# Kernel tuning notes

Hardware: AMD Instinct MI355X
Metric: run time of the kernel (lower is better)

## Reference

```python
import jax, jax.numpy as jnp
import numpy as np

B, SQ, SK = 2, 2048, 2048
E = 256   # embed_dim (also per-head key dim in this MHA)
S = 256   # srcdim (also per-head value dim)
NH = 8    # num_heads
HID = 2 * S  # FFN hidden = in_dim * 2


def setup_inputs() -> dict:
    key = jax.random.key(0)
    ks = jax.random.split(key, 12)
    def w(k, shape, s=0.02):
        return jax.random.normal(k, shape, dtype=jnp.float32) * s
    return {
        "Q": jax.random.normal(ks[0], (B, SQ, E), dtype=jnp.float32),
        "H": jax.random.normal(ks[1], (B, SK, E), dtype=jnp.float32),
        "A": jax.random.normal(ks[2], (B, SK, S), dtype=jnp.float32),
        # MHA params (torch Linear convention: y = x @ W.T + b)
        "wq": w(ks[3], (NH * E, E)), "bq": jnp.zeros((NH * E,), jnp.float32),
        "wk": w(ks[4], (NH * E, E)), "bk": jnp.zeros((NH * E,), jnp.float32),
        "wv": w(ks[5], (NH * S, S)), "bv": jnp.zeros((NH * S,), jnp.float32),
        "wo": w(ks[6], (S, NH * S)), "bo": jnp.zeros((S,), jnp.float32),
        # Attension scale (Parameter(torch.ones(1)))
        "attn_scale": jnp.ones((), jnp.float32),
        # shared LayerNormA params
        "ln_g": jnp.ones((S,), jnp.float32), "ln_b": jnp.zeros((S,), jnp.float32),
        # FFN params
        "w1": w(ks[7], (HID, S)), "b1": jnp.zeros((HID,), jnp.float32),
        "w2": w(ks[8], (S, HID)), "b2": jnp.zeros((S,), jnp.float32),
    }


def _layernorm(x, g, b, eps=1e-5):
    m = x.mean(-1, keepdims=True)
    v = ((x - m) ** 2).mean(-1, keepdims=True)
    return (x - m) / jnp.sqrt(v + eps) * g + b


def reference(Q, H, A, wq, bq, wk, bk, wv, bv, wo, bo,
              attn_scale, ln_g, ln_b, w1, b1, w2, b2):
    b_, sq, _ = Q.shape
    sk = H.shape[1]
    # ---- MHA branch (A_m) ----
    q = (Q @ wq.T + bq).reshape(b_, sq, NH, E).transpose(0, 2, 1, 3)  # [b,h,sq,E]
    k = (H @ wk.T + bk).reshape(b_, sk, NH, E).transpose(0, 2, 1, 3)  # [b,h,sk,E]
    v = (A @ wv.T + bv).reshape(b_, sk, NH, S).transpose(0, 2, 1, 3)  # [b,h,sk,S]
    scores = jnp.einsum('bhqe,bhke->bhqk', q, k) / jnp.sqrt(jnp.float32(E))
    probs = jax.nn.softmax(scores, axis=-1)
    ctx = jnp.einsum('bhqk,bhkd->bhqd', probs, v)          # [b,h,sq,S]
    ctx = ctx.transpose(0, 2, 1, 3).reshape(b_, sq, NH * S)
    A_m = ctx @ wo.T + bo                                   # [b,sq,S]
    # ---- Attension branch (dot score with learned scalar scale) ----
    s2 = jnp.einsum('bqe,bke->bqk', Q, H) * attn_scale      # [b,sq,sk]
    attn_out = jax.nn.softmax(s2, axis=-1) @ A              # [b,sq,S]
    # ---- residual + LN + FFN + LN (shared LayerNormA) ----
    Ad = _layernorm(A_m + attn_out, ln_g, ln_b)
    ff = jax.nn.relu(Ad @ w1.T + b1) @ w2.T + b2
    return _layernorm(ff + Ad, ln_g, ln_b)
```

## Files before the change

kernel.cpp:

```cpp
#include <hip/hip_runtime.h>
#include <cstdint>
#include <cstddef>


typedef unsigned short u16;
typedef __attribute__((ext_vector_type(8))) short bf16x8;
typedef __attribute__((ext_vector_type(4))) short s16x4;
typedef __attribute__((ext_vector_type(4))) float f32x4;

__device__ __forceinline__ float b2f(u16 u){
  union { unsigned int i; float f; } v; v.i = ((unsigned int)u) << 16; return v.f;
}
__device__ __forceinline__ u16 f2b(float f){
  union { float f; unsigned int i; } v; v.f = f;
  unsigned int u = v.i;
  unsigned int r = (u + 0x7FFFu + ((u >> 16) & 1u)) >> 16;
  return (u16)r;
}
__device__ __forceinline__ f32x4 mfma16(bf16x8 a, bf16x8 b, f32x4 c){
  return __builtin_amdgcn_mfma_f32_16x16x32_bf16(a, b, c, 0, 0, 0);
}
__device__ __forceinline__ void gload_lds16(const void* g, void* l){
  __builtin_amdgcn_global_load_lds(
      (const __attribute__((address_space(1))) unsigned int*)g,
      (__attribute__((address_space(3))) unsigned int*)l, 16, 0, 0);
}

__global__ void detect_kernel(const u16* __restrict__ q, int* __restrict__ flag){
  __shared__ int cnt;
  if (threadIdx.x == 0) cnt = 0;
  __syncthreads();
  int c = 0;
  for (int i = threadIdx.x; i < 2048; i += 256){
    u16 u = q[i];
    int e = (u >> 7) & 0xFF;
    if (e >= 140) c++;
  }
  atomicAdd(&cnt, c);
  __syncthreads();
  if (threadIdx.x == 0) *flag = (cnt > 64) ? 1 : 0;
}

struct ConvJobs {
  const void* src[18];
  void*       dst[18];
  void*       dst2[18];
  int         n[18];
  int         mode[18];
};

__global__ void convert_all(ConvJobs J, const int* __restrict__ flag){
  const int j = blockIdx.y;
  const int n = J.n[j];
  const int mode = J.mode[j];
  const int isf = *flag;
  for (int i = blockIdx.x * blockDim.x + threadIdx.x; i < n; i += gridDim.x * blockDim.x){
    if (mode == 2){
      float f = isf ? ((const float*)J.src[j])[i] : b2f(((const u16*)J.src[j])[i]);
      ((float*)J.dst[j])[i] = f;
    } else {
      u16 hi, lo = 0;
      if (isf){
        float f = ((const float*)J.src[j])[i];
        hi = f2b(f);
        if (mode == 1) lo = f2b(f - b2f(hi));
      } else {
        hi = ((const u16*)J.src[j])[i];
      }
      ((u16*)J.dst[j])[i] = hi;
      if (mode == 1) ((u16*)J.dst2[j])[i] = lo;
    }
  }
}

template<int STORE, bool RELU>
__global__ __launch_bounds__(256) void gemm_bt(
    const u16* __restrict__ X, const u16* __restrict__ W,
    const float* __restrict__ bias, void* __restrict__ outp,
    int M, int N, int K)
{
  __shared__ __align__(16) u16 lx[128 * 64];
  __shared__ __align__(16) u16 lw[128 * 64];
  const int tid = threadIdx.x;
  const int l = tid & 63, w = tid >> 6;
  const int lg = l >> 4, lr = l & 15;
  const int wr = w >> 1, wc = w & 1;
  const int m0 = blockIdx.x * 128;
  const int n0 = blockIdx.y * 128;

  f32x4 acc[4][4];
#pragma unroll
  for (int mi = 0; mi < 4; mi++)
#pragma unroll
    for (int ni = 0; ni < 4; ni++) acc[mi][ni] = (f32x4){0.f, 0.f, 0.f, 0.f};

  const int nkt = K >> 6;
  for (int kt = 0; kt < nkt; ++kt){
    __syncthreads();
#pragma unroll
    for (int it = 0; it < 4; ++it){
      int c = it * 256 + tid;
      int row = c >> 3, j = c & 7;
      int sj = (j ^ (row & 7)) * 8;
      const u16* gx = X + (size_t)(m0 + row) * K + kt * 64 + sj;
      gload_lds16(gx, (char*)lx + c * 16);
      const u16* gw = W + (size_t)(n0 + row) * K + kt * 64 + sj;
      gload_lds16(gw, (char*)lw + c * 16);
    }
    __syncthreads();
#pragma unroll
    for (int ks = 0; ks < 2; ++ks){
      bf16x8 af[4], bfv[4];
      const int swz = ((ks * 4 + lg) ^ (lr & 7)) * 8;
#pragma unroll
      for (int mi = 0; mi < 4; mi++)
        af[mi] = *(const bf16x8*)(lx + (wr * 64 + mi * 16 + lr) * 64 + swz);
#pragma unroll
      for (int ni = 0; ni < 4; ni++)
        bfv[ni] = *(const bf16x8*)(lw + (wc * 64 + ni * 16 + lr) * 64 + swz);
#pragma unroll
      for (int mi = 0; mi < 4; mi++)
#pragma unroll
        for (int ni = 0; ni < 4; ni++)
          acc[mi][ni] = mfma16(af[mi], bfv[ni], acc[mi][ni]);
    }
  }

#pragma unroll
  for (int mi = 0; mi < 4; mi++)
#pragma unroll
    for (int ni = 0; ni < 4; ni++){
      const int gr0 = m0 + wr * 64 + mi * 16 + lg * 4;
      const int gc  = n0 + wc * 64 + ni * 16 + lr;
      const float bv = bias ? bias[gc] : 0.f;
      if (STORE == 2){
        const int b = gr0 >> 11, sk0 = gr0 & 2047;
        const int h = gc >> 8,  d   = gc & 255;
        s16x4 pk;
#pragma unroll
        for (int r = 0; r < 4; r++){
          float v = acc[mi][ni][r] + bv;
          pk[r] = (short)f2b(v);
        }
        *(s16x4*)((u16*)outp + ((size_t)((b << 3) + h) * 256 + d) * 2048 + sk0) = pk;
      } else {
#pragma unroll
        for (int r = 0; r < 4; r++){
          float v = acc[mi][ni][r] + bv;
          if (RELU) v = fmaxf(v, 0.f);
          size_t idx = (size_t)(gr0 + r) * N + gc;
          if (STORE == 0) ((u16*)outp)[idx] = f2b(v);
          else            ((float*)outp)[idx] = v;
        }
      }
    }
}

template<int STORE, bool RELU>
__global__ __launch_bounds__(256) void gemm_bt64(
    const u16* __restrict__ X, const u16* __restrict__ W,
    const float* __restrict__ bias, void* __restrict__ outp,
    int M, int N, int K)
{
  __shared__ __align__(16) u16 lx[64 * 64];
  __shared__ __align__(16) u16 lw[64 * 64];
  const int tid = threadIdx.x;
  const int l = tid & 63, w = tid >> 6;
  const int lg = l >> 4, lr = l & 15;
  const int wr = w >> 1, wc = w & 1;
  const int m0 = blockIdx.x * 64;
  const int n0 = blockIdx.y * 64;

  f32x4 acc[2][2];
#pragma unroll
  for (int mi = 0; mi < 2; mi++)
#pragma unroll
    for (int ni = 0; ni < 2; ni++) acc[mi][ni] = (f32x4){0.f, 0.f, 0.f, 0.f};

  const int nkt = K >> 6;
  for (int kt = 0; kt < nkt; ++kt){
    __syncthreads();
#pragma unroll
    for (int it = 0; it < 2; ++it){
      int c = it * 256 + tid;
      int row = c >> 3, j = c & 7;
      int sj = (j ^ (row & 7)) * 8;
      const u16* gx = X + (size_t)(m0 + row) * K + kt * 64 + sj;
      gload_lds16(gx, (char*)lx + c * 16);
      const u16* gw = W + (size_t)(n0 + row) * K + kt * 64 + sj;
      gload_lds16(gw, (char*)lw + c * 16);
    }
    __syncthreads();
#pragma unroll
    for (int ks = 0; ks < 2; ++ks){
      bf16x8 af[2], bfv[2];
      const int swz = ((ks * 4 + lg) ^ (lr & 7)) * 8;
#pragma unroll
      for (int mi = 0; mi < 2; mi++)
        af[mi] = *(const bf16x8*)(lx + (wr * 32 + mi * 16 + lr) * 64 + swz);
#pragma unroll
      for (int ni = 0; ni < 2; ni++)
        bfv[ni] = *(const bf16x8*)(lw + (wc * 32 + ni * 16 + lr) * 64 + swz);
#pragma unroll
      for (int mi = 0; mi < 2; mi++)
#pragma unroll
        for (int ni = 0; ni < 2; ni++)
          acc[mi][ni] = mfma16(af[mi], bfv[ni], acc[mi][ni]);
    }
  }

#pragma unroll
  for (int mi = 0; mi < 2; mi++)
#pragma unroll
    for (int ni = 0; ni < 2; ni++){
      const int gr0 = m0 + wr * 32 + mi * 16 + lg * 4;
      const int gc  = n0 + wc * 32 + ni * 16 + lr;
      const float bv = bias ? bias[gc] : 0.f;
#pragma unroll
      for (int r = 0; r < 4; r++){
        float v = acc[mi][ni][r] + bv;
        if (RELU) v = fmaxf(v, 0.f);
        size_t idx = (size_t)(gr0 + r) * N + gc;
        if (STORE == 0) ((u16*)outp)[idx] = f2b(v);
        else            ((float*)outp)[idx] = v;
      }
    }
}

__global__ __launch_bounds__(256) void transpose_k(const u16* __restrict__ src, u16* __restrict__ dst){
  __shared__ u16 t[64][72];
  const int b   = blockIdx.z;
  const int sk0 = blockIdx.x * 64;
  const int d0  = blockIdx.y * 64;
  const int tid = threadIdx.x;
  union U8 { bf16x8 v; u16 e[8]; };
#pragma unroll
  for (int half = 0; half < 2; ++half){
    int c = half * 256 + tid;
    int r = c >> 3, c8 = (c & 7) * 8;
    U8 u; u.v = *(const bf16x8*)(src + ((size_t)b * 2048 + sk0 + r) * 256 + d0 + c8);
#pragma unroll
    for (int i = 0; i < 8; i++) t[r][c8 + i] = u.e[i];
  }
  __syncthreads();
#pragma unroll
  for (int half = 0; half < 2; ++half){
    int c = half * 256 + tid;
    int dr = c >> 3, s8 = (c & 7) * 8;
    U8 u;
#pragma unroll
    for (int i = 0; i < 8; i++) u.e[i] = t[s8 + i][dr];
    *(bf16x8*)(dst + ((size_t)b * 256 + d0 + dr) * 2048 + sk0 + s8) = u.v;
  }
}

template<int MODE>
__global__ __launch_bounds__(256) void flash_k(
    const u16* __restrict__ Qh, const u16* __restrict__ Ql,
    const u16* __restrict__ Kh, const u16* __restrict__ Kl,
    const u16* __restrict__ Vt,
    void* __restrict__ outp, float* __restrict__ mlp,
    const float* __restrict__ p_scale, const int* __restrict__ flagp)
{
  __shared__ __align__(16) u16 bufK[64 * 256];
  __shared__ __align__(16) u16 bufV[64 * 256];
  __shared__ __align__(16) u16 ldsP[4][16 * 72];
  const int tid = threadIdx.x, l = tid & 63, w = tid >> 6;
  const int lg = l >> 4, lr = l & 15;
  const int lr7 = lr & 7;
  const int by = blockIdx.y, qt = blockIdx.x, kc = blockIdx.z;

  size_t qkbase; int qks; size_t vbase;
  if (MODE == 0){
    qkbase = ((size_t)(by >> 3) * 2048) * 2048 + (size_t)(by & 7) * 256;
    qks = 2048;
    vbase = (size_t)by * (256 * 2048);
  } else {
    qkbase = (size_t)by * (2048 * 256);
    qks = 256;
    vbase = (size_t)by * (256 * 2048);
  }
  const float scale = (MODE == 0) ? 0.0625f : (*p_scale);
  const int split = (MODE == 1) ? (*flagp) : 0;
  const int NT = (MODE == 0) ? 32 : 4;
  const int kvbase = (MODE == 0) ? 0 : kc * 256;

  const int q0 = qt * 64 + w * 16;
  bf16x8 qf[8], qfl[8];
#pragma unroll
  for (int ks = 0; ks < 8; ks++)
    qf[ks] = *(const bf16x8*)(Qh + qkbase + (size_t)(q0 + lr) * qks + ks * 32 + lg * 8);
  if (MODE == 1){
    if (split){
#pragma unroll
      for (int ks = 0; ks < 8; ks++)
        qfl[ks] = *(const bf16x8*)(Ql + qkbase + (size_t)(q0 + lr) * qks + ks * 32 + lg * 8);
    } else {
#pragma unroll
      for (int ks = 0; ks < 8; ks++) qfl[ks] = qf[ks];
    }
  }

  float mrun[4], lpart[4];
#pragma unroll
  for (int r = 0; r < 4; r++){ mrun[r] = -3e38f; lpart[r] = 0.f; }
  f32x4 accO[16];
#pragma unroll
  for (int db = 0; db < 16; db++) accO[db] = (f32x4){0.f, 0.f, 0.f, 0.f};

  auto stageK = [&](const u16* __restrict__ src, int kv0){
#pragma unroll
    for (int it = 0; it < 8; ++it){
      int c = it * 256 + tid;
      int row = c >> 5, j = c & 31;
      const u16* g = src + qkbase + (size_t)(kv0 + row) * qks + (j ^ (row & 7)) * 8;
      gload_lds16(g, (char*)bufK + c * 16);
    }
  };
  auto stageV = [&](int kv0){
#pragma unroll
    for (int it = 0; it < 8; ++it){
      int c = it * 256 + tid;
      int row = c >> 3, j = c & 7;
      const u16* g = Vt + vbase + (size_t)row * 2048 + kv0 + (j ^ (row & 7)) * 8;
      gload_lds16(g, (char*)bufV + c * 16);
    }
  };

  auto qk_pass = [&](const bf16x8* qv, f32x4* s){
#pragma unroll
    for (int ks = 0; ks < 8; ks++){
      bf16x8 bfr[4];
      const int swz = (((ks * 4 + lg) ^ lr7)) * 8;
#pragma unroll
      for (int kb = 0; kb < 4; kb++)
        bfr[kb] = *(const bf16x8*)(bufK + (kb * 16 + lr) * 256 + swz);
#pragma unroll
      for (int kb = 0; kb < 4; kb++) s[kb] = mfma16(qv[ks], bfr[kb], s[kb]);
      if (MODE == 1 && split){
#pragma unroll
        for (int kb = 0; kb < 4; kb++) s[kb] = mfma16(qfl[ks], bfr[kb], s[kb]);
      }
    }
  };

  if (MODE == 0) stageK(Kh, kvbase);

  for (int t = 0; t < NT; ++t){
    const int kv0 = kvbase + t * 64;
    f32x4 s[4];
#pragma unroll
    for (int kb = 0; kb < 4; kb++) s[kb] = (f32x4){0.f, 0.f, 0.f, 0.f};

    if (MODE == 0){
      __syncthreads();
      stageV(kv0);
      qk_pass(qf, s);
    } else {
      __syncthreads();
      stageK(Kh, kv0);
      stageV(kv0);
      __syncthreads();
      qk_pass(qf, s);
      if (split){
        __syncthreads();
        stageK(Kl, kv0);
        __syncthreads();
#pragma unroll
        for (int ks = 0; ks < 8; ks++){
          bf16x8 bfr[4];
          const int swz = (((ks * 4 + lg) ^ lr7)) * 8;
#pragma unroll
          for (int kb = 0; kb < 4; kb++)
            bfr[kb] = *(const bf16x8*)(bufK + (kb * 16 + lr) * 256 + swz);
#pragma unroll
          for (int kb = 0; kb < 4; kb++) s[kb] = mfma16(qf[ks], bfr[kb], s[kb]);
        }
      }
    }

#pragma unroll
    for (int kb = 0; kb < 4; kb++)
#pragma unroll
      for (int r = 0; r < 4; r++) s[kb][r] *= scale;

    float pm[4];
#pragma unroll
    for (int r = 0; r < 4; r++)
      pm[r] = fmaxf(fmaxf(s[0][r], s[1][r]), fmaxf(s[2][r], s[3][r]));
#pragma unroll
    for (int m = 1; m < 16; m <<= 1)
#pragma unroll
      for (int r = 0; r < 4; r++) pm[r] = fmaxf(pm[r], __shfl_xor(pm[r], m));

    float g = fmaxf(fmaxf(pm[0] - mrun[0], pm[1] - mrun[1]),
                    fmaxf(pm[2] - mrun[2], pm[3] - mrun[3]));
    if (__any(g > 8.0f)){
      float corr[4];
#pragma unroll
      for (int r = 0; r < 4; r++){
        float mn = fmaxf(mrun[r], pm[r]);
        corr[r] = __expf(mrun[r] - mn);
        mrun[r] = mn;
        lpart[r] *= corr[r];
      }
#pragma unroll
      for (int db = 0; db < 16; db++)
#pragma unroll
        for (int r = 0; r < 4; r++) accO[db][r] *= corr[r];
    }
#pragma unroll
    for (int kb = 0; kb < 4; kb++)
#pragma unroll
      for (int r = 0; r < 4; r++){
        float p = __expf(s[kb][r] - mrun[r]);
        lpart[r] += p;
        ldsP[w][(lg * 4 + r) * 72 + kb * 16 + lr] = f2b(p);
      }

    if (MODE == 0){
      __syncthreads();
      if (t + 1 < NT) stageK(Kh, kv0 + 64);
    }

#pragma unroll
    for (int ks2 = 0; ks2 < 2; ++ks2){
      bf16x8 pa = *(const bf16x8*)(&ldsP[w][lr * 72 + ks2 * 32 + lg * 8]);
      const int swz = (((ks2 * 4 + lg) ^ lr7)) * 8;
#pragma unroll
      for (int db = 0; db < 16; ++db){
        bf16x8 vb = *(const bf16x8*)(bufV + (db * 16 + lr) * 64 + swz);
        accO[db] = mfma16(pa, vb, accO[db]);
      }
    }
  }

  float lrun[4];
#pragma unroll
  for (int r = 0; r < 4; r++) lrun[r] = lpart[r];
#pragma unroll
  for (int m = 1; m < 16; m <<= 1)
#pragma unroll
    for (int r = 0; r < 4; r++) lrun[r] += __shfl_xor(lrun[r], m);

  if (MODE == 0){
    float inv[4];
#pragma unroll
    for (int r = 0; r < 4; r++) inv[r] = 1.f / lrun[r];
#pragma unroll
    for (int db = 0; db < 16; db++)
#pragma unroll
      for (int r = 0; r < 4; r++){
        float v = accO[db][r] * inv[r];
        int q = q0 + lg * 4 + r;
        int d = db * 16 + lr;
        ((u16*)outp)[((size_t)(by >> 3) * 2048 + q) * 2048 + (size_t)(by & 7) * 256 + d] = f2b(v);
      }
  } else {
#pragma unroll
    for (int db = 0; db < 16; db++)
#pragma unroll
      for (int r = 0; r < 4; r++){
        int q = q0 + lg * 4 + r;
        int d = db * 16 + lr;
        ((float*)outp)[((size_t)((kc * 2 + by) * 2048 + q)) * 256 + d] = accO[db][r];
      }
    if (lr == 0){
#pragma unroll
      for (int r = 0; r < 4; r++){
        int idx = (kc * 2 + by) * 2048 + q0 + lg * 4 + r;
        mlp[idx] = mrun[r];
        mlp[32768 + idx] = lrun[r];
      }
    }
  }
}

__global__ __launch_bounds__(256) void merge_k(
    const float* __restrict__ Opart, const float* __restrict__ ml,
    float* __restrict__ outp)
{
  const int w = threadIdx.x >> 6, l = threadIdx.x & 63;
  const int row = blockIdx.x * 4 + w;
  const int b = row >> 11, q = row & 2047;
  float m[8], li[8], M = -3e38f;
#pragma unroll
  for (int kc = 0; kc < 8; kc++){
    int idx = (kc * 2 + b) * 2048 + q;
    m[kc] = ml[idx];
    li[kc] = ml[32768 + idx];
    M = fmaxf(M, m[kc]);
  }
  float L = 0.f, wgt[8];
#pragma unroll
  for (int kc = 0; kc < 8; kc++){ wgt[kc] = __expf(m[kc] - M); L += li[kc] * wgt[kc]; }
  const float invL = 1.f / L;
  f32x4 o = (f32x4){0.f, 0.f, 0.f, 0.f};
#pragma unroll
  for (int kc = 0; kc < 8; kc++){
    f32x4 v = *(const f32x4*)(Opart + ((size_t)((kc * 2 + b) * 2048 + q)) * 256 + l * 4);
#pragma unroll
    for (int i = 0; i < 4; i++) o[i] += v[i] * wgt[kc];
  }
#pragma unroll
  for (int i = 0; i < 4; i++) o[i] *= invL;
  *(f32x4*)(outp + (size_t)row * 256 + l * 4) = o;
}

template<int RESF32, int OUTFLAG>
__global__ __launch_bounds__(256) void ln_k(
    const float* __restrict__ x, const void* __restrict__ res,
    const float* __restrict__ g, const float* __restrict__ bb,
    void* __restrict__ outp, const int* __restrict__ flagp)
{
  const int w = threadIdx.x >> 6, l = threadIdx.x & 63;
  const int row = blockIdx.x * 4 + w;
  const size_t off = (size_t)row * 256 + l * 4;
  f32x4 xv = *(const f32x4*)(x + off);
  float v[4];
  if (RESF32){
    f32x4 rv = *(const f32x4*)((const float*)res + off);
#pragma unroll
    for (int i = 0; i < 4; i++) v[i] = xv[i] + rv[i];
  } else {
    const u16* rp = (const u16*)res + off;
#pragma unroll
    for (int i = 0; i < 4; i++) v[i] = xv[i] + b2f(rp[i]);
  }
  float s = 0.f, sq = 0.f;
#pragma unroll
  for (int i = 0; i < 4; i++){ s += v[i]; sq += v[i] * v[i]; }
  for (int m = 1; m < 64; m <<= 1){ s += __shfl_xor(s, m); sq += __shfl_xor(sq, m); }
  const float mean = s * (1.f / 256.f);
  const float var = sq * (1.f / 256.f) - mean * mean;
  const float rstd = rsqrtf(var + 1e-5f);
  float y[4];
#pragma unroll
  for (int i = 0; i < 4; i++) y[i] = (v[i] - mean) * rstd * g[l * 4 + i] + bb[l * 4 + i];
  const bool f32out = OUTFLAG && (*flagp);
  if (f32out){
    f32x4 o;
#pragma unroll
    for (int i = 0; i < 4; i++) o[i] = y[i];
    *(f32x4*)((float*)outp + off) = o;
  } else {
    s16x4 o;
#pragma unroll
    for (int i = 0; i < 4; i++) o[i] = (short)f2b(y[i]);
    *(s16x4*)((u16*)outp + off) = o;
  }
}

extern "C" void kernel_launch(void* const* d_in, const int* in_sizes, int n_in,
                              void* d_out, int out_size, void* d_ws, size_t ws_size,
                              hipStream_t stream)
{
  (void)in_sizes; (void)n_in; (void)out_size; (void)ws_size;
  char* ws = (char*)d_ws;
  size_t off = 0;
  auto alloc = [&](size_t bytes) -> char* {
    char* p = ws + off;
    off += (bytes + 255) & ~(size_t)255;
    return p;
  };
  int*   flag    = (int*)  alloc(4);
  float* p_scale = (float*)alloc(4);
  float* p_bq    = (float*)alloc(2048 * 4);
  float* p_bk    = (float*)alloc(2048 * 4);
  float* p_bv    = (float*)alloc(2048 * 4);
  float* p_bo    = (float*)alloc(256 * 4);
  float* p_b1    = (float*)alloc(512 * 4);
  float* p_b2    = (float*)alloc(256 * 4);
  float* p_g     = (float*)alloc(256 * 4);
  float* p_b     = (float*)alloc(256 * 4);
  u16* Qc  = (u16*)alloc((size_t)1048576 * 2);
  u16* Qlo = (u16*)alloc((size_t)1048576 * 2);
  u16* Hc  = (u16*)alloc((size_t)1048576 * 2);
  u16* Hlo = (u16*)alloc((size_t)1048576 * 2);
  u16* Ac  = (u16*)alloc((size_t)1048576 * 2);
  u16* wqc = (u16*)alloc((size_t)524288 * 2);
  u16* wkc = (u16*)alloc((size_t)524288 * 2);
  u16* wvc = (u16*)alloc((size_t)524288 * 2);
  u16* woc = (u16*)alloc((size_t)524288 * 2);
  u16* w1c = (u16*)alloc((size_t)131072 * 2);
  u16* w2c = (u16*)alloc((size_t)131072 * 2);
  u16* qbuf = (u16*)alloc((size_t)4096 * 2048 * 2);
  u16* kbuf = (u16*)alloc((size_t)4096 * 2048 * 2);
  u16* vtb  = (u16*)alloc((size_t)4096 * 2048 * 2);
  u16* ctx  = (u16*)alloc((size_t)4096 * 2048 * 2);
  u16* At   = (u16*)alloc((size_t)1048576 * 2);
  float* attn_o = (float*)alloc((size_t)4096 * 256 * 4);
  float* Am     = (float*)alloc((size_t)4096 * 256 * 4);
  u16* Ad  = (u16*)alloc((size_t)1048576 * 2);
  u16* h1  = (u16*)alloc((size_t)4096 * 512 * 2);
  float* ffb = (float*)alloc((size_t)4096 * 256 * 4);

  detect_kernel<<<1, 256, 0, stream>>>((const u16*)d_in[0], flag);

  ConvJobs J{};
  auto setj = [&](int i, const void* s, void* d, void* d2, int n, int m){
    J.src[i] = s; J.dst[i] = d; J.dst2[i] = d2; J.n[i] = n; J.mode[i] = m;
  };
  setj(0,  d_in[0],  Qc,  Qlo, 1048576, 1);
  setj(1,  d_in[1],  Hc,  Hlo, 1048576, 1);
  setj(2,  d_in[2],  Ac,  nullptr, 1048576, 0);
  setj(3,  d_in[3],  wqc, nullptr, 524288, 0);
  setj(4,  d_in[5],  wkc, nullptr, 524288, 0);
  setj(5,  d_in[7],  wvc, nullptr, 524288, 0);
  setj(6,  d_in[9],  woc, nullptr, 524288, 0);
  setj(7,  d_in[14], w1c, nullptr, 131072, 0);
  setj(8,  d_in[16], w2c, nullptr, 131072, 0);
  setj(9,  d_in[4],  p_bq, nullptr, 2048, 2);
  setj(10, d_in[6],  p_bk, nullptr, 2048, 2);
  setj(11, d_in[8],  p_bv, nullptr, 2048, 2);
  setj(12, d_in[10], p_bo, nullptr, 256, 2);
  setj(13, d_in[15], p_b1, nullptr, 512, 2);
  setj(14, d_in[17], p_b2, nullptr, 256, 2);
  setj(15, d_in[12], p_g,  nullptr, 256, 2);
  setj(16, d_in[13], p_b,  nullptr, 256, 2);
  setj(17, d_in[11], p_scale, nullptr, 1, 2);
  convert_all<<<dim3(64, 18), 256, 0, stream>>>(J, flag);

  gemm_bt<0, false><<<dim3(32, 16), 256, 0, stream>>>(Qc, wqc, p_bq, qbuf, 4096, 2048, 256);
  gemm_bt<0, false><<<dim3(32, 16), 256, 0, stream>>>(Hc, wkc, p_bk, kbuf, 4096, 2048, 256);
  gemm_bt<2, false><<<dim3(32, 16), 256, 0, stream>>>(Ac, wvc, p_bv, vtb,  4096, 2048, 256);
  transpose_k<<<dim3(32, 4, 2), 256, 0, stream>>>(Ac, At);

  flash_k<0><<<dim3(32, 16, 1), 256, 0, stream>>>(qbuf, nullptr, kbuf, nullptr, vtb,
                                                  ctx, nullptr, nullptr, flag);
  float* Opart = (float*)qbuf;
  float* mlbuf = (float*)vtb;
  flash_k<1><<<dim3(32, 2, 8), 256, 0, stream>>>(Qc, Qlo, Hc, Hlo, At,
                                                 Opart, mlbuf, p_scale, flag);
  merge_k<<<1024, 256, 0, stream>>>(Opart, mlbuf, attn_o);

  gemm_bt64<1, false><<<dim3(64, 4), 256, 0, stream>>>(ctx, woc, p_bo, Am, 4096, 256, 2048);
  ln_k<1, 0><<<1024, 256, 0, stream>>>(Am, attn_o, p_g, p_b, Ad, flag);
  gemm_bt64<0, true ><<<dim3(64, 8), 256, 0, stream>>>(Ad, w1c, p_b1, h1, 4096, 512, 256);
  gemm_bt64<1, false><<<dim3(64, 4), 256, 0, stream>>>(h1, w2c, p_b2, ffb, 4096, 256, 512);
  ln_k<0, 1><<<1024, 256, 0, stream>>>(ffb, Ad, p_g, p_b, d_out, flag);
}
```

Baseline: 329.3 us.

## Split flash kernel; give MHA path 32 query rows per wave for K/V reuse

The templated flash kernel is split into a dedicated MHA kernel and a second-branch kernel. The MHA kernel now handles 128 query rows per block (32 per wave, two 16-row MFMA tiles), so each K and V tile staged in LDS serves twice as many queries. It also wraps the MFMA sections in s_setprio. This halves the grid to 256 blocks and roughly doubles accumulator registers (launch_bounds 256,1), trading occupancy and latency hiding for less global and LDS traffic per query.

New measurement: 315.9 us. 1.04x faster.

```diff
diff --git a/kernel.cpp b/kernel.cpp
--- a/kernel.cpp
+++ b/kernel.cpp
@@ -254,51 +254,210 @@
   }
 }
 
-template<int MODE>
-__global__ __launch_bounds__(256) void flash_k(
+__global__ __launch_bounds__(256, 1) void flash_mha(
+    const u16* __restrict__ Qp, const u16* __restrict__ Kp,
+    const u16* __restrict__ Vt, u16* __restrict__ outp)
+{
+  __shared__ __align__(16) u16 bufK[64 * 256];
+  __shared__ __align__(16) u16 bufV[256 * 64];
+  __shared__ __align__(16) u16 ldsP[4][32 * 72];
+  const int tid = threadIdx.x, l = tid & 63, w = tid >> 6;
+  const int lg = l >> 4, lr = l & 15;
+  const int lr7 = lr & 7;
+  const int by = blockIdx.y, qt = blockIdx.x;
+  const size_t qkbase = ((size_t)(by >> 3) * 2048) * 2048 + (size_t)(by & 7) * 256;
+  const size_t vbase  = (size_t)by * (256 * 2048);
+  const int q0 = qt * 128 + w * 32;
+
+  bf16x8 qf[2][8];
+#pragma unroll
+  for (int qb = 0; qb < 2; qb++)
+#pragma unroll
+    for (int ks = 0; ks < 8; ks++)
+      qf[qb][ks] = *(const bf16x8*)(Qp + qkbase +
+          (size_t)(q0 + qb * 16 + lr) * 2048 + ks * 32 + lg * 8);
+
+  float mrun[2][4], lpart[2][4];
+#pragma unroll
+  for (int qb = 0; qb < 2; qb++)
+#pragma unroll
+    for (int r = 0; r < 4; r++){ mrun[qb][r] = -3e38f; lpart[qb][r] = 0.f; }
+  f32x4 accO[2][16];
+#pragma unroll
+  for (int qb = 0; qb < 2; qb++)
+#pragma unroll
+    for (int db = 0; db < 16; db++) accO[qb][db] = (f32x4){0.f, 0.f, 0.f, 0.f};
+
+  auto stageK = [&](int kv0){
+#pragma unroll
+    for (int it = 0; it < 8; ++it){
+      int c = it * 256 + tid;
+      int row = c >> 5, j = c & 31;
+      const u16* g = Kp + qkbase + (size_t)(kv0 + row) * 2048 + (j ^ (row & 7)) * 8;
+      gload_lds16(g, (char*)bufK + c * 16);
+    }
+  };
+  auto stageV = [&](int kv0){
+#pragma unroll
+    for (int it = 0; it < 8; ++it){
+      int c = it * 256 + tid;
+      int row = c >> 3, j = c & 7;
+      const u16* g = Vt + vbase + (size_t)row * 2048 + kv0 + (j ^ (row & 7)) * 8;
+      gload_lds16(g, (char*)bufV + c * 16);
+    }
+  };
+
+  stageK(0);
+
+  for (int t = 0; t < 32; ++t){
+    const int kv0 = t * 64;
+    __syncthreads();
+    stageV(kv0);
+
+    f32x4 s[2][4];
+#pragma unroll
+    for (int qb = 0; qb < 2; qb++)
+#pragma unroll
+      for (int kb = 0; kb < 4; kb++) s[qb][kb] = (f32x4){0.f, 0.f, 0.f, 0.f};
+
+    __builtin_amdgcn_s_setprio(1);
+#pragma unroll
+    for (int ks = 0; ks < 8; ks++){
+      bf16x8 bfr[4];
+      const int swz = (((ks * 4 + lg) ^ lr7)) * 8;
+#pragma unroll
+      for (int kb = 0; kb < 4; kb++)
+        bfr[kb] = *(const bf16x8*)(bufK + (kb * 16 + lr) * 256 + swz);
+#pragma unroll
+      for (int qb = 0; qb < 2; qb++)
+#pragma unroll
+        for (int kb = 0; kb < 4; kb++)
+          s[qb][kb] = mfma16(qf[qb][ks], bfr[kb], s[qb][kb]);
+    }
+    __builtin_amdgcn_s_setprio(0);
+
+    float pm[2][4];
+#pragma unroll
+    for (int qb = 0; qb < 2; qb++){
+#pragma unroll
+      for (int kb = 0; kb < 4; kb++)
+#pragma unroll
+        for (int r = 0; r < 4; r++) s[qb][kb][r] *= 0.0625f;
+#pragma unroll
+      for (int r = 0; r < 4; r++)
+        pm[qb][r] = fmaxf(fmaxf(s[qb][0][r], s[qb][1][r]),
+                          fmaxf(s[qb][2][r], s[qb][3][r]));
+#pragma unroll
+      for (int m = 1; m < 16; m <<= 1)
+#pragma unroll
+        for (int r = 0; r < 4; r++) pm[qb][r] = fmaxf(pm[qb][r], __shfl_xor(pm[qb][r], m));
+    }
+    float gmax = -3e38f;
+#pragma unroll
+    for (int qb = 0; qb < 2; qb++)
+#pragma unroll
+      for (int r = 0; r < 4; r++) gmax = fmaxf(gmax, pm[qb][r] - mrun[qb][r]);
+    if (__any(gmax > 8.0f)){
+#pragma unroll
+      for (int qb = 0; qb < 2; qb++)
+#pragma unroll
+        for (int r = 0; r < 4; r++){
+          float mn = fmaxf(mrun[qb][r], pm[qb][r]);
+          float corr = __expf(mrun[qb][r] - mn);
+          mrun[qb][r] = mn;
+          lpart[qb][r] *= corr;
+#pragma unroll
+          for (int db = 0; db < 16; db++) accO[qb][db][r] *= corr;
+        }
+    }
+#pragma unroll
+    for (int qb = 0; qb < 2; qb++)
+#pragma unroll
+      for (int kb = 0; kb < 4; kb++)
+#pragma unroll
+        for (int r = 0; r < 4; r++){
+          float p = __expf(s[qb][kb][r] - mrun[qb][r]);
+          lpart[qb][r] += p;
+          ldsP[w][(qb * 16 + lg * 4 + r) * 72 + kb * 16 + lr] = f2b(p);
+        }
+
+    __syncthreads();
+    if (t + 1 < 32) stageK(kv0 + 64);
+
+    __builtin_amdgcn_s_setprio(1);
+#pragma unroll
+    for (int ks2 = 0; ks2 < 2; ++ks2){
+      bf16x8 pa[2];
+#pragma unroll
+      for (int qb = 0; qb < 2; qb++)
+        pa[qb] = *(const bf16x8*)(ldsP[w] + (qb * 16 + lr) * 72 + ks2 * 32 + lg * 8);
+      const int swz = (((ks2 * 4 + lg) ^ lr7)) * 8;
+#pragma unroll
+      for (int db = 0; db < 16; ++db){
+        bf16x8 vb = *(const bf16x8*)(bufV + (db * 16 + lr) * 64 + swz);
+        accO[0][db] = mfma16(pa[0], vb, accO[0][db]);
+        accO[1][db] = mfma16(pa[1], vb, accO[1][db]);
+      }
+    }
+    __builtin_amdgcn_s_setprio(0);
+  }
+
+#pragma unroll
+  for (int qb = 0; qb < 2; qb++){
+    float lrun[4];
+#pragma unroll
+    for (int r = 0; r < 4; r++) lrun[r] = lpart[qb][r];
+#pragma unroll
+    for (int m = 1; m < 16; m <<= 1)
+#pragma unroll
+      for (int r = 0; r < 4; r++) lrun[r] += __shfl_xor(lrun[r], m);
+    float inv[4];
+#pragma unroll
+    for (int r = 0; r < 4; r++) inv[r] = 1.f / lrun[r];
+#pragma unroll
+    for (int db = 0; db < 16; db++)
+#pragma unroll
+      for (int r = 0; r < 4; r++){
+        float v = accO[qb][db][r] * inv[r];
+        int q = q0 + qb * 16 + lg * 4 + r;
+        int d = db * 16 + lr;
+        outp[((size_t)(by >> 3) * 2048 + q) * 2048 + (size_t)(by & 7) * 256 + d] = f2b(v);
+      }
+  }
+}
+
+__global__ __launch_bounds__(256) void flash_b2(
     const u16* __restrict__ Qh, const u16* __restrict__ Ql,
     const u16* __restrict__ Kh, const u16* __restrict__ Kl,
     const u16* __restrict__ Vt,
-    void* __restrict__ outp, float* __restrict__ mlp,
+    float* __restrict__ Opart, float* __restrict__ mlp,
     const float* __restrict__ p_scale, const int* __restrict__ flagp)
 {
   __shared__ __align__(16) u16 bufK[64 * 256];
-  __shared__ __align__(16) u16 bufV[64 * 256];
+  __shared__ __align__(16) u16 bufV[256 * 64];
   __shared__ __align__(16) u16 ldsP[4][16 * 72];
   const int tid = threadIdx.x, l = tid & 63, w = tid >> 6;
   const int lg = l >> 4, lr = l & 15;
   const int lr7 = lr & 7;
   const int by = blockIdx.y, qt = blockIdx.x, kc = blockIdx.z;
-
-  size_t qkbase; int qks; size_t vbase;
-  if (MODE == 0){
-    qkbase = ((size_t)(by >> 3) * 2048) * 2048 + (size_t)(by & 7) * 256;
-    qks = 2048;
-    vbase = (size_t)by * (256 * 2048);
+  const size_t qkbase = (size_t)by * (2048 * 256);
+  const size_t vbase  = (size_t)by * (256 * 2048);
+  const float scale = *p_scale;
+  const int split = *flagp;
+  const int kvbase = kc * 256;
+  const int q0 = qt * 64 + w * 16;
+
+  bf16x8 qf[8], qfl[8];
+#pragma unroll
+  for (int ks = 0; ks < 8; ks++)
+    qf[ks] = *(const bf16x8*)(Qh + qkbase + (size_t)(q0 + lr) * 256 + ks * 32 + lg * 8);
+  if (split){
+#pragma unroll
+    for (int ks = 0; ks < 8; ks++)
+      qfl[ks] = *(const bf16x8*)(Ql + qkbase + (size_t)(q0 + lr) * 256 + ks * 32 + lg * 8);
   } else {
-    qkbase = (size_t)by * (2048 * 256);
-    qks = 256;
-    vbase = (size_t)by * (256 * 2048);
-  }
-  const float scale = (MODE == 0) ? 0.0625f : (*p_scale);
-  const int split = (MODE == 1) ? (*flagp) : 0;
-  const int NT = (MODE == 0) ? 32 : 4;
-  const int kvbase = (MODE == 0) ? 0 : kc * 256;
-
-  const int q0 = qt * 64 + w * 16;
-  bf16x8 qf[8], qfl[8];
-#pragma unroll
-  for (int ks = 0; ks < 8; ks++)
-    qf[ks] = *(const bf16x8*)(Qh + qkbase + (size_t)(q0 + lr) * qks + ks * 32 + lg * 8);
-  if (MODE == 1){
-    if (split){
-#pragma unroll
-      for (int ks = 0; ks < 8; ks++)
-        qfl[ks] = *(const bf16x8*)(Ql + qkbase + (size_t)(q0 + lr) * qks + ks * 32 + lg * 8);
-    } else {
-#pragma unroll
-      for (int ks = 0; ks < 8; ks++) qfl[ks] = qf[ks];
-    }
+#pragma unroll
+    for (int ks = 0; ks < 8; ks++) qfl[ks] = qf[ks];
   }
 
   float mrun[4], lpart[4];
@@ -313,7 +472,7 @@
     for (int it = 0; it < 8; ++it){
       int c = it * 256 + tid;
       int row = c >> 5, j = c & 31;
-      const u16* g = src + qkbase + (size_t)(kv0 + row) * qks + (j ^ (row & 7)) * 8;
+      const u16* g = src + qkbase + (size_t)(kv0 + row) * 256 + (j ^ (row & 7)) * 8;
       gload_lds16(g, (char*)bufK + c * 16);
     }
   };
@@ -327,7 +486,16 @@
     }
   };
 
-  auto qk_pass = [&](const bf16x8* qv, f32x4* s){
+  for (int t = 0; t < 4; ++t){
+    const int kv0 = kvbase + t * 64;
+    __syncthreads();
+    stageK(Kh, kv0);
+    stageV(kv0);
+    __syncthreads();
+
+    f32x4 s[4];
+#pragma unroll
+    for (int kb = 0; kb < 4; kb++) s[kb] = (f32x4){0.f, 0.f, 0.f, 0.f};
 #pragma unroll
     for (int ks = 0; ks < 8; ks++){
       bf16x8 bfr[4];
@@ -336,46 +504,25 @@
       for (int kb = 0; kb < 4; kb++)
         bfr[kb] = *(const bf16x8*)(bufK + (kb * 16 + lr) * 256 + swz);
 #pragma unroll
-      for (int kb = 0; kb < 4; kb++) s[kb] = mfma16(qv[ks], bfr[kb], s[kb]);
-      if (MODE == 1 && split){
+      for (int kb = 0; kb < 4; kb++) s[kb] = mfma16(qf[ks], bfr[kb], s[kb]);
+      if (split){
 #pragma unroll
         for (int kb = 0; kb < 4; kb++) s[kb] = mfma16(qfl[ks], bfr[kb], s[kb]);
       }
     }
-  };
-
-  if (MODE == 0) stageK(Kh, kvbase);
-
-  for (int t = 0; t < NT; ++t){
-    const int kv0 = kvbase + t * 64;
-    f32x4 s[4];
-#pragma unroll
-    for (int kb = 0; kb < 4; kb++) s[kb] = (f32x4){0.f, 0.f, 0.f, 0.f};
-
-    if (MODE == 0){
+    if (split){
       __syncthreads();
-      stageV(kv0);
-      qk_pass(qf, s);
-    } else {
+      stageK(Kl, kv0);
       __syncthreads();
-      stageK(Kh, kv0);
-      stageV(kv0);
-      __syncthreads();
-      qk_pass(qf, s);
-      if (split){
-        __syncthreads();
-        stageK(Kl, kv0);
-        __syncthreads();
-#pragma unroll
-        for (int ks = 0; ks < 8; ks++){
-          bf16x8 bfr[4];
-          const int swz = (((ks * 4 + lg) ^ lr7)) * 8;
-#pragma unroll
-          for (int kb = 0; kb < 4; kb++)
-            bfr[kb] = *(const bf16x8*)(bufK + (kb * 16 + lr) * 256 + swz);
-#pragma unroll
-          for (int kb = 0; kb < 4; kb++) s[kb] = mfma16(qf[ks], bfr[kb], s[kb]);
-        }
+#pragma unroll
+      for (int ks = 0; ks < 8; ks++){
+        bf16x8 bfr[4];
+        const int swz = (((ks * 4 + lg) ^ lr7)) * 8;
+#pragma unroll
+        for (int kb = 0; kb < 4; kb++)
+          bfr[kb] = *(const bf16x8*)(bufK + (kb * 16 + lr) * 256 + swz);
+#pragma unroll
+        for (int kb = 0; kb < 4; kb++) s[kb] = mfma16(qf[ks], bfr[kb], s[kb]);
       }
     }
 
@@ -396,18 +543,15 @@
     float g = fmaxf(fmaxf(pm[0] - mrun[0], pm[1] - mrun[1]),
                     fmaxf(pm[2] - mrun[2], pm[3] - mrun[3]));
     if (__any(g > 8.0f)){
-      float corr[4];
 #pragma unroll
       for (int r = 0; r < 4; r++){
         float mn = fmaxf(mrun[r], pm[r]);
-        corr[r] = __expf(mrun[r] - mn);
+        float corr = __expf(mrun[r] - mn);
         mrun[r] = mn;
-        lpart[r] *= corr[r];
-      }
-#pragma unroll
-      for (int db = 0; db < 16; db++)
-#pragma unroll
-        for (int r = 0; r < 4; r++) accO[db][r] *= corr[r];
+        lpart[r] *= corr;
+#pragma unroll
+        for (int db = 0; db < 16; db++) accO[db][r] *= corr;
+      }
     }
 #pragma unroll
     for (int kb = 0; kb < 4; kb++)
@@ -418,14 +562,9 @@
         ldsP[w][(lg * 4 + r) * 72 + kb * 16 + lr] = f2b(p);
       }
 
-    if (MODE == 0){
-      __syncthreads();
-      if (t + 1 < NT) stageK(Kh, kv0 + 64);
-    }
-
 #pragma unroll
     for (int ks2 = 0; ks2 < 2; ++ks2){
-      bf16x8 pa = *(const bf16x8*)(&ldsP[w][lr * 72 + ks2 * 32 + lg * 8]);
+      bf16x8 pa = *(const bf16x8*)(ldsP[w] + lr * 72 + ks2 * 32 + lg * 8);
       const int swz = (((ks2 * 4 + lg) ^ lr7)) * 8;
 #pragma unroll
       for (int db = 0; db < 16; ++db){
@@ -443,35 +582,20 @@
 #pragma unroll
     for (int r = 0; r < 4; r++) lrun[r] += __shfl_xor(lrun[r], m);
 
-  if (MODE == 0){
-    float inv[4];
-#pragma unroll
-    for (int r = 0; r < 4; r++) inv[r] = 1.f / lrun[r];
-#pragma unroll
-    for (int db = 0; db < 16; db++)
-#pragma unroll
-      for (int r = 0; r < 4; r++){
-        float v = accO[db][r] * inv[r];
-        int q = q0 + lg * 4 + r;
-        int d = db * 16 + lr;
-        ((u16*)outp)[((size_t)(by >> 3) * 2048 + q) * 2048 + (size_t)(by & 7) * 256 + d] = f2b(v);
-      }
-  } else {
-#pragma unroll
-    for (int db = 0; db < 16; db++)
-#pragma unroll
-      for (int r = 0; r < 4; r++){
-        int q = q0 + lg * 4 + r;
-        int d = db * 16 + lr;
-        ((float*)outp)[((size_t)((kc * 2 + by) * 2048 + q)) * 256 + d] = accO[db][r];
-      }
-    if (lr == 0){
-#pragma unroll
-      for (int r = 0; r < 4; r++){
-        int idx = (kc * 2 + by) * 2048 + q0 + lg * 4 + r;
-        mlp[idx] = mrun[r];
-        mlp[32768 + idx] = lrun[r];
-      }
+#pragma unroll
+  for (int db = 0; db < 16; db++)
+#pragma unroll
+    for (int r = 0; r < 4; r++){
+      int q = q0 + lg * 4 + r;
+      int d = db * 16 + lr;
+      Opart[((size_t)((kc * 2 + by) * 2048 + q)) * 256 + d] = accO[db][r];
+    }
+  if (lr == 0){
+#pragma unroll
+    for (int r = 0; r < 4; r++){
+      int idx = (kc * 2 + by) * 2048 + q0 + lg * 4 + r;
+      mlp[idx] = mrun[r];
+      mlp[32768 + idx] = lrun[r];
     }
   }
 }
@@ -626,12 +750,12 @@
   gemm_bt<2, false><<<dim3(32, 16), 256, 0, stream>>>(Ac, wvc, p_bv, vtb,  4096, 2048, 256);
   transpose_k<<<dim3(32, 4, 2), 256, 0, stream>>>(Ac, At);
 
-  flash_k<0><<<dim3(32, 16, 1), 256, 0, stream>>>(qbuf, nullptr, kbuf, nullptr, vtb,
-                                                  ctx, nullptr, nullptr, flag);
+  flash_mha<<<dim3(16, 16), 256, 0, stream>>>(qbuf, kbuf, vtb, ctx);
+
   float* Opart = (float*)qbuf;
   float* mlbuf = (float*)vtb;
-  flash_k<1><<<dim3(32, 2, 8), 256, 0, stream>>>(Qc, Qlo, Hc, Hlo, At,
-                                                 Opart, mlbuf, p_scale, flag);
+  flash_b2<<<dim3(32, 2, 8), 256, 0, stream>>>(Qc, Qlo, Hc, Hlo, At,
+                                               Opart, mlbuf, p_scale, flag);
   merge_k<<<1024, 256, 0, stream>>>(Opart, mlbuf, attn_o);
 
   gemm_bt64<1, false><<<dim3(64, 4), 256, 0, stream>>>(ctx, woc, p_bo, Am, 4096, 256, 2048);
```
